# Kernel tuning notes

Hardware: AMD Instinct MI355X
Metric: run time of the kernel (lower is better)

## Reference

```python
import jax, jax.numpy as jnp
import numpy as np

D_MODEL = 1024
H = 4
DK = 128   # head_qk_dim (key_dim=512)
DV = 256   # head_v_dim (value_dim=1024)
EPS = 1e-5
SCALE = DK ** -0.5


def setup_inputs() -> dict:
    key = jax.random.key(0)
    ks = jax.random.split(key, 8)
    w = lambda k, i, o: jax.random.normal(k, (i, o), jnp.float32) * (2.0 ** -2.5) * (6.0 / (i + o)) ** 0.5 * 2
    return {
        "x": jax.random.normal(ks[0], (2, 4096, D_MODEL), jnp.float32),
        "Wq": w(ks[1], D_MODEL, H * DK),
        "Wk": w(ks[2], D_MODEL, H * DK),
        "Wv": w(ks[3], D_MODEL, H * DV),
        "Wb": w(ks[4], D_MODEL, H),
        "Wg": w(ks[5], D_MODEL, H * DV),
        "Wo": w(ks[6], H * DV, D_MODEL),
        "norm_w": jnp.ones((DV,), jnp.float32),
    }


def _delta_rule(q, k, v, beta):
    """Delta-rule linear attention. q,k: [b,n,h,dk], v: [b,n,h,dv], beta: [b,n,h].
    S_t = S_{t-1} + k_t (beta_t * (v_t - k_t^T S_{t-1}))^T ; o_t = q_t^T S_t."""
    b = q.shape[0]
    # time-major for scan: [n,b,h,*]
    qt = jnp.moveaxis(q, 1, 0)
    kt = jnp.moveaxis(k, 1, 0)
    vt = jnp.moveaxis(v, 1, 0)
    bt = jnp.moveaxis(beta, 1, 0)
    S0 = jnp.zeros((b, H, DK, DV), q.dtype)

    def step(S, inp):
        q_t, k_t, v_t, b_t = inp
        pred = jnp.einsum('bhk,bhkv->bhv', k_t, S)          # current memory readout
        delta = (v_t - pred) * b_t[..., None]                # beta-scaled error
        S = S + k_t[..., :, None] * delta[..., None, :]      # rank-1 update [b,h,dk,dv]
        o_t = jnp.einsum('bhk,bhkv->bhv', q_t, S)
        return S, o_t

    _, o = jax.lax.scan(step, S0, (qt, kt, vt, bt))          # o: [n,b,h,dv]
    return jnp.moveaxis(o, 0, 1)                             # [b,n,h,dv]


def reference(x, Wq, Wk, Wv, Wb, Wg, Wo, norm_w):
    b, n, _ = x.shape
    q = (x @ Wq).reshape(b, n, H, DK)
    k = (x @ Wk).reshape(b, n, H, DK)
    v = (x @ Wv).reshape(b, n, H, DV)
    beta = jax.nn.sigmoid(x @ Wb)                            # [b,n,h]
    # L2-normalize keys (delta-rule kernels assume unit-norm k) and scale q
    k = k * jax.lax.rsqrt(jnp.sum(k * k, axis=-1, keepdims=True) + 1e-12)
    q = q * SCALE
    o = _delta_rule(q, k, v, beta)                           # [b,n,h,dv]
    # FusedRMSNormSwishGate over head_v_dim
    g = (x @ Wg).reshape(b, n, H, DV)
    o = o * jax.lax.rsqrt(jnp.mean(o * o, axis=-1, keepdims=True) + EPS) * norm_w
    o = o * (g * jax.nn.sigmoid(g))                          # swish gate
    return o.reshape(b, n, H * DV) @ Wo
```

## Files before the change

kernel.cpp:

```cpp
#include <hip/hip_runtime.h>
#include <hip/hip_bf16.h>
#include <stdint.h>
#include <stddef.h>

typedef __attribute__((ext_vector_type(8))) short short8v;
typedef __attribute__((ext_vector_type(4))) float f32x4;
typedef unsigned short us;

__device__ __forceinline__ float bf2f(unsigned short u) {
    return __uint_as_float(((unsigned int)u) << 16);
}
__device__ __forceinline__ unsigned short f2bf(float f) {
    unsigned int x = __float_as_uint(f);
    x += 0x7fffu + ((x >> 16) & 1u);
    return (unsigned short)(x >> 16);
}
__device__ __forceinline__ unsigned int cvtpk(float lo, float hi) {
    unsigned int r;
    asm("v_cvt_pk_bf16_f32 %0, %1, %2" : "=v"(r) : "v"(lo), "v"(hi));
    return r;
}

#define NTOK 8192
#define DM   1024
#define NPROJ 3072
#define SEQ  4096
#define NCHUNK 64
#define SCQ 0.08838834764831845f

#define GLDS16(g, l) __builtin_amdgcn_global_load_lds( \
    (const __attribute__((address_space(1))) void*)(g), \
    (__attribute__((address_space(3))) void*)(l), 16, 0, 0)

__device__ __forceinline__ void bar_lgkm() {
    asm volatile("s_waitcnt lgkmcnt(0)" ::: "memory");
    __builtin_amdgcn_s_barrier();
    __builtin_amdgcn_sched_barrier(0);
}

__device__ __forceinline__ int sw16(int row, int k) {
    int u = k >> 3;
    int us_ = (u & 8) | ((u ^ row) & 7);
    return row * 128 + us_ * 8 + (k & 7);
}
__device__ __forceinline__ int sw8(int row, int k) {
    int u = k >> 3;
    int us_ = (u ^ row) & 7;
    return row * 64 + us_ * 8 + (k & 7);
}
__device__ __forceinline__ int sw128(int row, int k) {
    int u = k >> 3;
    return row * 128 + ((u ^ row) & 15) * 8 + (k & 7);
}
__device__ __forceinline__ int sw64(int row, int k) {
    int u = k >> 3;
    return row * 64 + ((u ^ row) & 7) * 8 + (k & 7);
}
__device__ __forceinline__ int sw64b(int row, int k) {
    int u = k >> 3;
    return row * 64 + ((u ^ row ^ (row >> 3)) & 7) * 8 + (k & 7);
}
__device__ __forceinline__ int swU(int t, int j) {
    int jj = j & 127, u = jj >> 3;
    int us_ = (u & 8) | ((u ^ t) & 7);
    return t * 256 + (j >> 7) * 128 + us_ * 8 + (jj & 7);
}
__device__ __forceinline__ int swU128(int t, int jj) {
    int u = jj >> 3;
    int us_ = (u & 8) | ((u ^ t) & 7);
    return t * 128 + us_ * 8 + (jj & 7);
}

__global__ __launch_bounds__(256) void prep(
    const float* __restrict__ x, us* __restrict__ xb,
    const float* __restrict__ Wb, float* __restrict__ beta,
    const float* __restrict__ Wq, const float* __restrict__ Wk,
    const float* __restrict__ Wv, const float* __restrict__ Wg,
    const float* __restrict__ Wo, us* __restrict__ WT, us* __restrict__ WoT)
{
    __shared__ float smem[64 * 65];
    int tid = threadIdx.x;
    int bid = blockIdx.x;

    if (bid < 4096) {
        int i = bid * 256 + tid;
        int tok = i >> 7;
        int kb = (i >> 3) & 15;
        int u = i & 7;
        int ko = kb * 64 + ((u ^ (tok & 7)) * 8);
        const float4* src = (const float4*)(x + (size_t)tok * 1024 + ko);
        float4 v0 = src[0], v1 = src[1];
        uint4 o;
        o.x = cvtpk(v0.x, v0.y); o.y = cvtpk(v0.z, v0.w);
        o.z = cvtpk(v1.x, v1.y); o.w = cvtpk(v1.z, v1.w);
        *(uint4*)(xb + (size_t)i * 8) = o;
        const float4* wbv = (const float4*)Wb;
        float xs[8] = {v0.x, v0.y, v0.z, v0.w, v1.x, v1.y, v1.z, v1.w};
        float4 s = {0.f, 0.f, 0.f, 0.f};
        #pragma unroll
        for (int e = 0; e < 8; e++) {
            float4 w = wbv[ko + e];
            s.x += xs[e] * w.x; s.y += xs[e] * w.y;
            s.z += xs[e] * w.z; s.w += xs[e] * w.w;
        }
        *(float4*)&smem[tid * 4] = s;
        __syncthreads();
        if (tid < 8) {
            int tp = tid >> 2, h = tid & 3;
            float acc = 0.f;
            for (int j = 0; j < 128; j++) acc += smem[(tp * 128 + j) * 4 + h];
            beta[(size_t)(bid * 2 + tp) * 4 + h] = 1.f / (1.f + __expf(-acc));
        }
        return;
    }

    int lb = bid - 4096;
    const float* srcw; us* dst; int N;
    if (lb < 128)      { srcw = Wq; dst = WT;                    N = 512;  }
    else if (lb < 256) { srcw = Wk; dst = WT + (size_t)512 * DM;  N = 512;  lb -= 128; }
    else if (lb < 512) { srcw = Wv; dst = WT + (size_t)1024 * DM; N = 1024; lb -= 256; }
    else if (lb < 768) { srcw = Wg; dst = WT + (size_t)2048 * DM; N = 1024; lb -= 512; }
    else               { srcw = Wo; dst = WoT;                   N = 1024; lb -= 768; }
    int nbx = N >> 6;
    int n0 = (lb % nbx) * 64, k0 = (lb / nbx) * 64;
    float (*tl)[65] = (float(*)[65])smem;
    int tr = tid >> 6, tc = tid & 63;
    #pragma unroll
    for (int i2 = 0; i2 < 16; i2++) {
        int kk = 4 * i2 + tr;
        tl[kk][tc] = srcw[(size_t)(k0 + kk) * N + n0 + tc];
    }
    __syncthreads();
    int n = tid >> 2, seg = (tid & 3) * 16;
    short8v a, b;
    #pragma unroll
    for (int e = 0; e < 8; e++) {
        a[e] = (short)f2bf(tl[seg + e][n]);
        b[e] = (short)f2bf(tl[seg + 8 + e][n]);
    }
    int n_ = n0 + n;
    int o1 = (tid & 3) * 2, o2_ = o1 + 1;
    us* d = dst + (size_t)n_ * DM + k0;
    *(short8v*)(d + (o1 ^ (n_ & 7)) * 8) = a;
    *(short8v*)(d + (o2_ ^ (n_ & 7)) * 8) = b;
}

template<int OUT_F32>
__global__ __launch_bounds__(256) void gemm_bt(
    const us* __restrict__ A, const us* __restrict__ BT,
    void* __restrict__ C, int M, int N, int K)
{
    __shared__ us As[2][128 * 64];
    __shared__ us Bs[2][128 * 64];
    int tid = threadIdx.x;
    int wave = tid >> 6, lane = tid & 63;
    int wr = (wave >> 1) * 64, wc = (wave & 1) * 64;
    int fr = lane & 15, fq = lane >> 4;
    int nbx = gridDim.x, nwg = nbx * gridDim.y;
    int wg = blockIdx.y * nbx + blockIdx.x;
    int cpx = nwg >> 3;
    wg = (wg & 7) * cpx + (wg >> 3);
    int m0 = (wg % nbx) * 128, n0 = (wg / nbx) * 128;

    f32x4 acc[4][4];
    #pragma unroll
    for (int i = 0; i < 4; i++)
        #pragma unroll
        for (int j = 0; j < 4; j++) acc[i][j] = (f32x4){0.f, 0.f, 0.f, 0.f};

    int rl = lane >> 3, ul = lane & 7;

    auto issue = [&](int k0, int bufi) {
        #pragma unroll
        for (int i = 0; i < 4; i++) {
            int row = wave * 32 + i * 8 + rl;
            GLDS16(&A[(size_t)(m0 + row) * K + k0 + ul * 8], &As[bufi][(wave * 32 + i * 8) * 64]);
            GLDS16(&BT[(size_t)(n0 + row) * K + k0 + ul * 8], &Bs[bufi][(wave * 32 + i * 8) * 64]);
        }
    };

    int NT = K >> 6;
    issue(0, 0);
    if (NT > 1) issue(64, 1);

    for (int t = 0; t < NT; t++) {
        if (t + 1 < NT) asm volatile("s_waitcnt vmcnt(8)" ::: "memory");
        else            asm volatile("s_waitcnt vmcnt(0)" ::: "memory");
        __builtin_amdgcn_sched_barrier(0);
        __builtin_amdgcn_s_barrier();
        __builtin_amdgcn_sched_barrier(0);
        const us* as = As[t & 1];
        const us* bs = Bs[t & 1];
        #pragma unroll
        for (int kk = 0; kk < 2; kk++) {
            short8v a[4], b[4];
            #pragma unroll
            for (int i = 0; i < 4; i++) {
                int ra = wr + i * 16 + fr;
                a[i] = *(const short8v*)&as[ra * 64 + ((4 * kk + fq) ^ (ra & 7)) * 8];
                int rb = wc + i * 16 + fr;
                b[i] = *(const short8v*)&bs[rb * 64 + ((4 * kk + fq) ^ (rb & 7)) * 8];
            }
            #pragma unroll
            for (int i = 0; i < 4; i++)
                #pragma unroll
                for (int j = 0; j < 4; j++)
                    acc[i][j] = __builtin_amdgcn_mfma_f32_16x16x32_bf16(a[i], b[j], acc[i][j], 0, 0, 0);
        }
        bar_lgkm();
        if (t + 2 < NT) issue((t + 2) * 64, t & 1);
    }

    #pragma unroll
    for (int i = 0; i < 4; i++)
        #pragma unroll
        for (int j = 0; j < 4; j++)
            #pragma unroll
            for (int t = 0; t < 4; t++) {
                int row = m0 + wr + i * 16 + fq * 4 + t;
                int col = n0 + wc + j * 16 + fr;
                float val = acc[i][j][t];
                if (OUT_F32) ((float*)C)[(size_t)row * N + col] = val;
                else ((us*)C)[(size_t)row * N + col] = f2bf(val);
            }
}

__global__ __launch_bounds__(256) void chunk_pre(
    const us* __restrict__ QKVG, const float* __restrict__ beta,
    us* __restrict__ Wbuf, us* __restrict__ Ubuf,
    us* __restrict__ Kbuf, us* __restrict__ KTbuf)
{
    __shared__ us Ks[8192];
    __shared__ us KTs[8192];
    __shared__ us VT[8192];
    __shared__ us Tb[4096];
    __shared__ float Af[64][64];
    __shared__ float betas[64];

    int c = blockIdx.x, bh = blockIdx.y;
    int b = bh >> 2, h = bh & 3;
    int tid = threadIdx.x;
    int wv = tid >> 6, ln = tid & 63;
    int fr = ln & 15, fq = ln >> 4;
    int tok0 = b * SEQ + c * 64;
    size_t cb = (size_t)bh * NCHUNK + c;

    #pragma unroll
    for (int r = 0; r < 4; r++) {
        int idx = tid + 256 * r;
        int t = idx >> 4, u = idx & 15;
        short8v kv = *(const short8v*)(QKVG + (size_t)(tok0 + t) * NPROJ + 512 + h * 128 + u * 8);
        *(short8v*)(Ks + sw16(t, u * 8)) = kv;
    }
    if (tid < 64) betas[tid] = beta[(size_t)(tok0 + tid) * 4 + h];
    __syncthreads();

    {
        int t = tid >> 2, p = tid & 3;
        short8v v[4];
        float ss = 0.f;
        #pragma unroll
        for (int uu = 0; uu < 4; uu++) {
            v[uu] = *(const short8v*)(Ks + sw16(t, (p * 4 + uu) * 8));
            #pragma unroll
            for (int e = 0; e < 8; e++) {
                float f = bf2f((unsigned short)v[uu][e]);
                ss += f * f;
            }
        }
        ss += __shfl_xor(ss, 1);
        ss += __shfl_xor(ss, 2);
        float rn = rsqrtf(ss + 1e-12f);
        #pragma unroll
        for (int uu = 0; uu < 4; uu++) {
            short8v o;
            #pragma unroll
            for (int e = 0; e < 8; e++)
                o[e] = (short)f2bf(bf2f((unsigned short)v[uu][e]) * rn);
            *(short8v*)(Ks + sw16(t, (p * 4 + uu) * 8)) = o;
        }
    }
    __syncthreads();

    {
        f32x4 aacc[4];
        #pragma unroll
        for (int jt = 0; jt < 4; jt++) aacc[jt] = (f32x4){0.f, 0.f, 0.f, 0.f};
        #pragma unroll
        for (int ks = 0; ks < 4; ks++) {
            short8v ak = *(const short8v*)(Ks + sw16(16 * wv + fr, 32 * ks + 8 * fq));
            #pragma unroll
            for (int jt = 0; jt < 4; jt++) {
                short8v bk = *(const short8v*)(Ks + sw16(16 * jt + fr, 32 * ks + 8 * fq));
                aacc[jt] = __builtin_amdgcn_mfma_f32_16x16x32_bf16(ak, bk, aacc[jt], 0, 0, 0);
            }
        }
        #pragma unroll
        for (int jt = 0; jt < 4; jt++)
            #pragma unroll
            for (int r = 0; r < 4; r++) {
                int t = 16 * wv + 4 * fq + r, s = 16 * jt + fr;
                if (s < t) Af[t][s] = betas[t] * aacc[jt][r];
            }
    }
    __syncthreads();

    if (wv == 0) {
        int cc = ln;
        for (int tb = 0; tb < 8; tb++) {
            int base = tb * 8;
            float xs[8];
            #pragma unroll
            for (int i = 0; i < 8; i++) {
                int t = base + i;
                float v = Af[t][cc];
                #pragma unroll
                for (int s = 0; s < i; s++)
                    v += Af[t][base + s] * xs[s];
                float xt = (cc < t) ? -v : 0.f;
                xs[i] = xt;
                if (cc < t) Af[t][cc] = xt;
            }
            for (int r = base + 8; r < 64; r += 2) {
                float u0 = 0.f, u1 = 0.f;
                #pragma unroll
                for (int s = 0; s < 8; s++) {
                    float a0 = Af[r][base + s];
                    float a1 = Af[r + 1][base + s];
                    u0 += a0 * xs[s];
                    u1 += a1 * xs[s];
                }
                Af[r][cc] += u0;
                Af[r + 1][cc] += u1;
            }
        }
    } else {
        int q = tid - 64;
        for (int g = q; g < 1024; g += 192) {
            int t = g >> 4, u = g & 15;
            short8v kv = *(const short8v*)(Ks + sw16(t, u * 8));
            #pragma unroll
            for (int e = 0; e < 8; e++)
                KTs[sw64b(u * 8 + e, t)] = (unsigned short)kv[e];
        }
        for (int g = q; g < 1024; g += 192) {
            int t = g >> 4, jg = g & 15;
            short8v vv = *(const short8v*)(QKVG + (size_t)(tok0 + t) * NPROJ + 1024 + h * 256 + jg * 8);
            #pragma unroll
            for (int e = 0; e < 8; e++)
                VT[sw64b(jg * 8 + e, t)] = (unsigned short)vv[e];
        }
    }
    __syncthreads();

    {
        #pragma unroll
        for (int i = 0; i < 4; i++) {
            int idx = tid + 256 * i;
            int t = idx >> 4, u = idx & 15;
            short8v kv = *(const short8v*)(Ks + sw16(t, u * 8));
            *(short8v*)(Kbuf + cb * 8192 + t * 128 + (size_t)(((u ^ t) & 15) * 8)) = kv;
        }
        #pragma unroll
        for (int i = 0; i < 16; i++) {
            int idx = tid + 256 * i;
            int t = idx >> 6, s = idx & 63;
            float tv = (s < t) ? Af[t][s] : (s == t ? 1.f : 0.f);
            Tb[sw8(t, s)] = f2bf(tv * betas[s]);
        }
        #pragma unroll
        for (int i = 0; i < 4; i++) {
            int idx = tid + 256 * i;
            *(short8v*)(KTbuf + cb * 8192 + (size_t)idx * 8) =
                *(const short8v*)(KTs + (size_t)idx * 8);
        }
    }
    __syncthreads();

    {
        f32x4 wacc[8], uacc[8];
        #pragma unroll
        for (int jt = 0; jt < 8; jt++) {
            wacc[jt] = (f32x4){0.f, 0.f, 0.f, 0.f};
            uacc[jt] = (f32x4){0.f, 0.f, 0.f, 0.f};
        }
        #pragma unroll
        for (int ks = 0; ks < 2; ks++) {
            short8v at = *(const short8v*)(Tb + sw8(16 * wv + fr, 32 * ks + 8 * fq));
            #pragma unroll
            for (int jt = 0; jt < 8; jt++) {
                short8v bk = *(const short8v*)(KTs + sw64b(16 * jt + fr, 32 * ks + 8 * fq));
                wacc[jt] = __builtin_amdgcn_mfma_f32_16x16x32_bf16(at, bk, wacc[jt], 0, 0, 0);
                short8v bv = *(const short8v*)(VT + sw64b(16 * jt + fr, 32 * ks + 8 * fq));
                uacc[jt] = __builtin_amdgcn_mfma_f32_16x16x32_bf16(at, bv, uacc[jt], 0, 0, 0);
            }
        }
        #pragma unroll
        for (int jt = 0; jt < 8; jt++)
            #pragma unroll
            for (int r = 0; r < 4; r++) {
                int t = 16 * wv + 4 * fq + r, d = 16 * jt + fr;
                Wbuf[cb * 8192 + (d >> 6) * 4096 + sw64(t, d & 63)] = f2bf(-wacc[jt][r]);
                Ubuf[cb * 16384 + swU(t, d)] = f2bf(uacc[jt][r]);
            }
    }
    __syncthreads();

    #pragma unroll
    for (int i = 0; i < 4; i++) {
        int g = tid + 256 * i;
        int t = g >> 4, jg = g & 15;
        short8v vv = *(const short8v*)(QKVG + (size_t)(tok0 + t) * NPROJ + 1024 + h * 256 + 128 + jg * 8);
        #pragma unroll
        for (int e = 0; e < 8; e++)
            VT[sw64b(jg * 8 + e, t)] = (unsigned short)vv[e];
    }
    __syncthreads();
    {
        f32x4 uacc[8];
        #pragma unroll
        for (int jt = 0; jt < 8; jt++) uacc[jt] = (f32x4){0.f, 0.f, 0.f, 0.f};
        #pragma unroll
        for (int ks = 0; ks < 2; ks++) {
            short8v at = *(const short8v*)(Tb + sw8(16 * wv + fr, 32 * ks + 8 * fq));
            #pragma unroll
            for (int jt = 0; jt < 8; jt++) {
                short8v bv = *(const short8v*)(VT + sw64b(16 * jt + fr, 32 * ks + 8 * fq));
                uacc[jt] = __builtin_amdgcn_mfma_f32_16x16x32_bf16(at, bv, uacc[jt], 0, 0, 0);
            }
        }
        #pragma unroll
        for (int jt = 0; jt < 8; jt++)
            #pragma unroll
            for (int r = 0; r < 4; r++) {
                int t = 16 * wv + 4 * fq + r, j = 16 * jt + fr;
                Ubuf[cb * 16384 + swU(t, 128 + j)] = f2bf(uacc[jt][r]);
            }
    }
}

#define SCW 0
#define SCKT 8192
#define SCU 16384
#define SCBUF 17408
#define SSTB (2 * SCBUF)
#define SDTB (2 * SCBUF + 2048)

__global__ __launch_bounds__(256, 1) void fused_scan_qg(
    const us* __restrict__ xb, const us* __restrict__ WT, us* __restrict__ QKVG,
    const us* __restrict__ Wbuf, const us* __restrict__ Ubuf,
    const us* __restrict__ KTbuf, us* __restrict__ Sbuf)
{
    extern __shared__ us lds[];
    int tid = threadIdx.x;

    if (blockIdx.x < 128) {
        if (tid >= 128) {
            for (int c = 0; c < NCHUNK; c++) __builtin_amdgcn_s_barrier();
            return;
        }
        int wv = tid >> 6, ln = tid & 63;
        int fr = ln & 15, fq = ln >> 4;
        int sl = blockIdx.x >> 3;
        int j0 = sl * 16;
        int bh = blockIdx.x & 7;

        short8v id0;
        #pragma unroll
        for (int e = 0; e < 8; e++)
            id0[e] = (short)((8 * fq + e == fr) ? 0x3F80 : 0);

        f32x4 sacc[4];
        #pragma unroll
        for (int i = 0; i < 4; i++) sacc[i] = (f32x4){0.f, 0.f, 0.f, 0.f};

        us* ST = lds + SSTB + wv * 1024;

        auto issue = [&](int c1) {
            size_t cb = (size_t)bh * NCHUNK + c1;
            us* dst = lds + (c1 & 1) * SCBUF;
            const us* Wc = Wbuf + cb * 8192 + wv * 4096;
            const us* Kc = KTbuf + cb * 8192 + wv * 4096;
            #pragma unroll
            for (int i = 0; i < 8; i++) {
                GLDS16(Wc + i * 512 + ln * 8, dst + SCW + wv * 4096 + i * 512);
                GLDS16(Kc + i * 512 + ln * 8, dst + SCKT + wv * 4096 + i * 512);
            }
            if (wv) {
                const us* Uc = Ubuf + cb * 16384;
                #pragma unroll
                for (int i = 0; i < 2; i++) {
                    int t = i * 32 + (ln >> 1);
                    GLDS16(Uc + swU(t, j0 + (ln & 1) * 8), dst + SCU + i * 512);
                }
            }
        };

        issue(0);

        for (int c = 0; c < NCHUNK; c++) {
            const us* ba = lds + (c & 1) * SCBUF;
            us* DTw = lds + SDTB + (c & 1) * 2048 + wv * 1024;
            const us* DTr = lds + SDTB + (c & 1) * 2048;
            size_t sb = ((size_t)bh * NCHUNK + c) * 32768 + sl * 2048 + wv * 1024;

            #pragma unroll
            for (int dt = 0; dt < 4; dt++) {
                uint2 w;
                w.x = cvtpk(sacc[dt][0], sacc[dt][1]);
                w.y = cvtpk(sacc[dt][2], sacc[dt][3]);
                int dl = 16 * dt + 4 * fq;
                int off = fr * 64 + (((dl >> 3) ^ fr) & 7) * 8 + (dl & 7);
                *(uint2*)&ST[off] = w;
                *(uint2*)(Sbuf + sb + off) = w;
            }
            if (c + 1 < NCHUNK) issue(c + 1);
            if (c + 1 < NCHUNK) {
                if (wv) asm volatile("s_waitcnt vmcnt(22)" ::: "memory");
                else    asm volatile("s_waitcnt vmcnt(20)" ::: "memory");
            } else {
                asm volatile("s_waitcnt vmcnt(4)" ::: "memory");
            }
            __builtin_amdgcn_sched_barrier(0);

            f32x4 dacc[4];
            #pragma unroll
            for (int tt = 0; tt < 4; tt++) dacc[tt] = (f32x4){0.f, 0.f, 0.f, 0.f};
            #pragma unroll
            for (int kc = 0; kc < 2; kc++) {
                short8v bs = *(const short8v*)&ST[fr * 64 + (((4 * kc + fq) ^ fr) & 7) * 8];
                #pragma unroll
                for (int tt = 0; tt < 4; tt++) {
                    short8v aw = *(const short8v*)&ba[SCW + wv * 4096 + sw64(16 * tt + fr, 32 * kc + 8 * fq)];
                    dacc[tt] = __builtin_amdgcn_mfma_f32_16x16x32_bf16(aw, bs, dacc[tt], 0, 0, 0);
                }
            }
            if (wv) {
                #pragma unroll
                for (int tt = 0; tt < 4; tt++) {
                    short8v au = *(const short8v*)&ba[SCU + (16 * tt + fr) * 16 + 8 * (fq & 1)];
                    dacc[tt] = __builtin_amdgcn_mfma_f32_16x16x32_bf16(au, id0, dacc[tt], 0, 0, 0);
                }
            }
            #pragma unroll
            for (int tt = 0; tt < 4; tt++) {
                uint2 w;
                w.x = cvtpk(dacc[tt][0], dacc[tt][1]);
                w.y = cvtpk(dacc[tt][2], dacc[tt][3]);
                int tl = 16 * tt + 4 * fq;
                *(uint2*)&DTw[fr * 64 + (((tl >> 3) ^ fr) & 7) * 8 + (tl & 7)] = w;
            }
            bar_lgkm();
            #pragma unroll
            for (int kc2 = 0; kc2 < 2; kc2++) {
                int o = fr * 64 + (((4 * kc2 + fq) ^ fr) & 7) * 8;
                short8v bd0 = *(const short8v*)&DTr[o];
                short8v bd1 = *(const short8v*)&DTr[1024 + o];
                #pragma unroll
                for (int dt = 0; dt < 4; dt++) {
                    short8v ak = *(const short8v*)&ba[SCKT + sw64b(64 * wv + 16 * dt + fr, 32 * kc2 + 8 * fq)];
                    sacc[dt] = __builtin_amdgcn_mfma_f32_16x16x32_bf16(ak, bd0, sacc[dt], 0, 0, 0);
                    sacc[dt] = __builtin_amdgcn_mfma_f32_16x16x32_bf16(ak, bd1, sacc[dt], 0, 0, 0);
                }
            }
        }
        return;
    }

    {
        us* As = lds;
        us* Bs = lds + 8192;
        int wave = tid >> 6, lane = tid & 63;
        int wr = (wave >> 1) * 64, wc = (wave & 1) * 64;
        int fr = lane & 15, fq = lane >> 4;
        int wg = blockIdx.x - 128;
        wg = (wg & 7) * 96 + (wg >> 3);
        int m0 = (wg % 64) * 128;
        int ntile = wg / 64;
        int n0 = ntile * 128 + (ntile >= 4 ? 1536 : 0);

        f32x4 acc[4][4];
        #pragma unroll
        for (int i = 0; i < 4; i++)
            #pragma unroll
            for (int j = 0; j < 4; j++) acc[i][j] = (f32x4){0.f, 0.f, 0.f, 0.f};

        int rl = lane >> 3, ul = lane & 7;

        for (int k0 = 0; k0 < DM; k0 += 64) {
            #pragma unroll
            for (int i = 0; i < 4; i++) {
                int row = wave * 32 + i * 8 + rl;
                GLDS16(&xb[(size_t)(m0 + row) * DM + k0 + ul * 8], As + (wave * 32 + i * 8) * 64);
                GLDS16(&WT[(size_t)(n0 + row) * DM + k0 + ul * 8], Bs + (wave * 32 + i * 8) * 64);
            }
            __syncthreads();
            #pragma unroll
            for (int kk = 0; kk < 2; kk++) {
                short8v a[4], b[4];
                #pragma unroll
                for (int i = 0; i < 4; i++) {
                    int ra = wr + i * 16 + fr;
                    a[i] = *(const short8v*)&As[ra * 64 + ((4 * kk + fq) ^ (ra & 7)) * 8];
                    int rb = wc + i * 16 + fr;
                    b[i] = *(const short8v*)&Bs[rb * 64 + ((4 * kk + fq) ^ (rb & 7)) * 8];
                }
                #pragma unroll
                for (int i = 0; i < 4; i++)
                    #pragma unroll
                    for (int j = 0; j < 4; j++)
                        acc[i][j] = __builtin_amdgcn_mfma_f32_16x16x32_bf16(a[i], b[j], acc[i][j], 0, 0, 0);
            }
            __syncthreads();
        }
        #pragma unroll
        for (int i = 0; i < 4; i++)
            #pragma unroll
            for (int j = 0; j < 4; j++)
                #pragma unroll
                for (int t = 0; t < 4; t++) {
                    int row = m0 + wr + i * 16 + fq * 4 + t;
                    int col = n0 + wc + j * 16 + fr;
                    QKVG[(size_t)row * NPROJ + col] = f2bf(acc[i][j][t]);
                }
    }
}

#define K2_W 0
#define K2_P 8192
#define K2_U 12288
#define K2_S 20480
#define K2_Q 36864
#define K2_DT 45056
#define K2_K 53248

__global__ __launch_bounds__(256, 1) void out_k(
    const us* __restrict__ QKVG, const us* __restrict__ Wbuf,
    const us* __restrict__ Ubuf, const us* __restrict__ Kbuf,
    const us* __restrict__ Sbuf, us* __restrict__ Ob)
{
    extern __shared__ us lds[];
    int tid = threadIdx.x;
    int wv = tid >> 6, ln = tid & 63;
    int fr = ln & 15, fq = ln >> 4;
    int c = blockIdx.x;
    int bh = blockIdx.y >> 1, jh = blockIdx.y & 1;
    int b = bh >> 2, h = bh & 3;
    int tok0 = b * SEQ + c * 64;
    size_t cb = (size_t)bh * NCHUNK + c;

    short8v id0, id1;
    #pragma unroll
    for (int e = 0; e < 8; e++) {
        id0[e] = (short)((8 * fq + e == fr) ? 0x3F80 : 0);
        id1[e] = (short)((8 * fq + e == fr + 16) ? 0x3F80 : 0);
    }

    #pragma unroll
    for (int i = 0; i < 4; i++) {
        int q = (i * 4 + wv) * 512 + ln * 8;
        GLDS16(Wbuf + cb * 8192 + q, lds + K2_W + (i * 4 + wv) * 512);
    }
    #pragma unroll
    for (int i = 0; i < 4; i++) {
        int q = (i * 4 + wv) * 512 + ln * 8;
        GLDS16(Kbuf + cb * 8192 + q, lds + K2_K + (i * 4 + wv) * 512);
    }
    #pragma unroll
    for (int i = 0; i < 4; i++) {
        int q = (i * 4 + wv) * 512 + ln * 8;
        int t = q >> 7, r = q & 127;
        GLDS16(Ubuf + cb * 16384 + t * 256 + jh * 128 + r, lds + K2_U + (i * 4 + wv) * 512);
    }
    size_t sbase = cb * 32768 + (size_t)jh * 16384;
    #pragma unroll
    for (int i = 0; i < 8; i++) {
        int q = (i * 4 + wv) * 512 + ln * 8;
        GLDS16(Sbuf + sbase + q, lds + K2_S + (i * 4 + wv) * 512);
    }
    short8v qv[4];
    #pragma unroll
    for (int i = 0; i < 4; i++) {
        int idx = tid + 256 * i;
        int t = idx >> 4, u = idx & 15;
        qv[i] = *(const short8v*)(QKVG + (size_t)(tok0 + t) * NPROJ + h * 128 + u * 8);
    }
    #pragma unroll
    for (int i = 0; i < 4; i++) {
        int idx = tid + 256 * i;
        int t = idx >> 4, u = idx & 15;
        *(short8v*)&lds[K2_Q + sw128(t, u * 8)] = qv[i];
    }
    __syncthreads();

    f32x4 dacc[8], oacc[8];
    #pragma unroll
    for (int jt = 0; jt < 8; jt++) {
        dacc[jt] = (f32x4){0.f, 0.f, 0.f, 0.f};
        oacc[jt] = (f32x4){0.f, 0.f, 0.f, 0.f};
    }
    #pragma unroll
    for (int ks = 0; ks < 4; ks++) {
        short8v aw = *(const short8v*)&lds[K2_W + (ks >> 1) * 4096
            + sw64(16 * wv + fr, (ks & 1) * 32 + 8 * fq)];
        short8v aq = *(const short8v*)&lds[K2_Q + sw128(16 * wv + fr, 32 * ks + 8 * fq)];
        #pragma unroll
        for (int jt = 0; jt < 8; jt++) {
            short8v bs = *(const short8v*)&lds[K2_S + jt * 2048 + (ks >> 1) * 1024
                + fr * 64 + ((((ks & 1) * 4 + fq) ^ fr) & 7) * 8];
            dacc[jt] = __builtin_amdgcn_mfma_f32_16x16x32_bf16(aw, bs, dacc[jt], 0, 0, 0);
            oacc[jt] = __builtin_amdgcn_mfma_f32_16x16x32_bf16(aq, bs, oacc[jt], 0, 0, 0);
        }
    }
    #pragma unroll
    for (int ju = 0; ju < 4; ju++) {
        short8v au = *(const short8v*)&lds[K2_U + swU128(16 * wv + fr, 32 * ju + 8 * fq)];
        dacc[2 * ju + 0] = __builtin_amdgcn_mfma_f32_16x16x32_bf16(au, id0, dacc[2 * ju + 0], 0, 0, 0);
        dacc[2 * ju + 1] = __builtin_amdgcn_mfma_f32_16x16x32_bf16(au, id1, dacc[2 * ju + 1], 0, 0, 0);
    }
    {
        f32x4 pacc[4];
        #pragma unroll
        for (int jt2 = 0; jt2 < 4; jt2++) pacc[jt2] = (f32x4){0.f, 0.f, 0.f, 0.f};
        #pragma unroll
        for (int ks = 0; ks < 4; ks++) {
            short8v aq = *(const short8v*)&lds[K2_Q + sw128(16 * wv + fr, 32 * ks + 8 * fq)];
            #pragma unroll
            for (int jt2 = 0; jt2 < 4; jt2++) {
                short8v bk = *(const short8v*)&lds[K2_K + sw128(16 * jt2 + fr, 32 * ks + 8 * fq)];
                pacc[jt2] = __builtin_amdgcn_mfma_f32_16x16x32_bf16(aq, bk, pacc[jt2], 0, 0, 0);
            }
        }
        #pragma unroll
        for (int jt2 = 0; jt2 < 4; jt2++)
            #pragma unroll
            for (int r = 0; r < 4; r++) {
                int t = 16 * wv + 4 * fq + r, s = 16 * jt2 + fr;
                float val = (s <= t) ? pacc[jt2][r] * SCQ : 0.f;
                lds[K2_P + sw64(t, s)] = f2bf(val);
            }
    }
    #pragma unroll
    for (int jt = 0; jt < 8; jt++)
        #pragma unroll
        for (int r = 0; r < 4; r++) oacc[jt][r] *= SCQ;
    #pragma unroll
    for (int jt = 0; jt < 8; jt++) {
        int j = 16 * jt + fr;
        int t0 = 16 * wv + 4 * fq;
        uint2 w;
        w.x = cvtpk(dacc[jt][0], dacc[jt][1]);
        w.y = cvtpk(dacc[jt][2], dacc[jt][3]);
        *(uint2*)&lds[K2_DT + sw64(j, t0)] = w;
    }
    bar_lgkm();

    #pragma unroll
    for (int ks = 0; ks < 2; ks++) {
        short8v ap = *(const short8v*)&lds[K2_P + sw64(16 * wv + fr, 32 * ks + 8 * fq)];
        #pragma unroll
        for (int jt = 0; jt < 8; jt++) {
            short8v bd = *(const short8v*)&lds[K2_DT + sw64(16 * jt + fr, 32 * ks + 8 * fq)];
            oacc[jt] = __builtin_amdgcn_mfma_f32_16x16x32_bf16(ap, bd, oacc[jt], 0, 0, 0);
        }
    }
    us* ob = Ob + (size_t)tok0 * 1024 + h * 256 + jh * 128;
    #pragma unroll
    for (int jt = 0; jt < 8; jt++)
        #pragma unroll
        for (int r = 0; r < 4; r++) {
            int t = 16 * wv + 4 * fq + r;
            ob[(size_t)t * 1024 + 16 * jt + fr] = f2bf(oacc[jt][r]);
        }
}

__global__ __launch_bounds__(256) void gate_norm(const us* __restrict__ Ob,
                                                 const us* __restrict__ QKVG,
                                                 const float* __restrict__ norm_w,
                                                 us* __restrict__ o2)
{
    int gid = blockIdx.x * 4 + (threadIdx.x >> 6);
    int ln = threadIdx.x & 63;
    int tok = gid >> 2, h = gid & 3;
    size_t base = (size_t)tok * 1024 + h * 256 + ln * 4;
    uint2 ov = *(const uint2*)&Ob[base];
    float o0 = bf2f((us)ov.x), o1 = bf2f((us)(ov.x >> 16));
    float o2v = bf2f((us)ov.y), o3 = bf2f((us)(ov.y >> 16));
    float ss = o0 * o0 + o1 * o1 + o2v * o2v + o3 * o3;
    #pragma unroll
    for (int off = 32; off; off >>= 1) ss += __shfl_xor(ss, off);
    float r = rsqrtf(ss * (1.0f / 256.0f) + 1e-5f);
    uint2 gv = *(const uint2*)&QKVG[(size_t)tok * NPROJ + 2048 + h * 256 + ln * 4];
    float g0 = bf2f((us)gv.x), g1 = bf2f((us)(gv.x >> 16));
    float g2 = bf2f((us)gv.y), g3 = bf2f((us)(gv.y >> 16));
    float4 nw = *(const float4*)&norm_w[ln * 4];
    float r0 = o0 * r * nw.x * (g0 / (1.f + __expf(-g0)));
    float r1 = o1 * r * nw.y * (g1 / (1.f + __expf(-g1)));
    float r2 = o2v * r * nw.z * (g2 / (1.f + __expf(-g2)));
    float r3 = o3 * r * nw.w * (g3 / (1.f + __expf(-g3)));
    uint2 w;
    w.x = cvtpk(r0, r1);
    w.y = cvtpk(r2, r3);
    int u = h * 32 + (ln >> 1);
    size_t dsto = (size_t)tok * 1024 + (size_t)(u >> 3) * 64
                + (size_t)(((u & 7) ^ (tok & 7)) * 8) + (ln & 1) * 4;
    *(uint2*)&o2[dsto] = w;
}

extern "C" void kernel_launch(void* const* d_in, const int* in_sizes, int n_in,
                              void* d_out, int out_size, void* d_ws, size_t ws_size,
                              hipStream_t stream) {
    const float* x      = (const float*)d_in[0];
    const float* Wq     = (const float*)d_in[1];
    const float* Wk     = (const float*)d_in[2];
    const float* Wv     = (const float*)d_in[3];
    const float* Wb     = (const float*)d_in[4];
    const float* Wg     = (const float*)d_in[5];
    const float* Wo     = (const float*)d_in[6];
    const float* norm_w = (const float*)d_in[7];
    float* out = (float*)d_out;

    char* ws = (char*)d_ws;
    us*    xb   = (us*)(ws + 0);
    us*    Ob   = (us*)(ws + 0);
    us*    WT   = (us*)(ws + 16777216);
    us*    KTbuf= (us*)(ws + 23068672);
    us*    QKVG = (us*)(ws + 31457280);
    float* beta = (float*)(ws + 81788928);
    us*    Wbuf = (us*)(ws + 81920000);
    us*    Ubuf = (us*)(ws + 90308608);
    us*    o2   = (us*)(ws + 90308608);
    us*    Kbuf = (us*)(ws + 107085824);
    us*    WoT  = (us*)(ws + 115474432);
    us*    Sbuf = (us*)(ws + 117571584);

    (void)hipFuncSetAttribute((const void*)fused_scan_qg,
                              hipFuncAttributeMaxDynamicSharedMemorySize, 81920);
    (void)hipFuncSetAttribute((const void*)out_k,
                              hipFuncAttributeMaxDynamicSharedMemorySize, 122880);

    prep<<<5120, 256, 0, stream>>>(x, xb, Wb, beta, Wq, Wk, Wv, Wg, Wo, WT, WoT);
    gemm_bt<0><<<dim3(64, 12), 256, 0, stream>>>(xb, WT + (size_t)512 * DM,
                                                 (void*)(QKVG + 512), NTOK, NPROJ, DM);
    chunk_pre<<<dim3(NCHUNK, 8), 256, 0, stream>>>(QKVG, beta, Wbuf, Ubuf, Kbuf, KTbuf);
    fused_scan_qg<<<896, 256, 81920, stream>>>(xb, WT, QKVG, Wbuf, Ubuf, KTbuf, Sbuf);
    out_k<<<dim3(NCHUNK, 16), 256, 122880, stream>>>(QKVG, Wbuf, Ubuf, Kbuf, Sbuf, Ob);
    gate_norm<<<NTOK, 256, 0, stream>>>(Ob, QKVG, norm_w, o2);
    gemm_bt<1><<<dim3(64, 8), 256, 0, stream>>>(o2, WoT, (void*)out, NTOK, DM, DM);
}
```

Before: 234.1 us.

## Fuse RMSNorm swish-gate into chunk output kernel with 512-thread blocks

Merges the two value-half blocks of out_k into one 512-thread block per (chunk, head), so W, K and the Q·K^T intra-chunk scores are loaded and computed once rather than twice. The per-token RMSNorm and swish gate, previously a separate gate_norm kernel, now run in the same block: output rows are staged as fp32 in LDS and the gate values are pulled in with async copies. This removes one launch and the bf16 Ob round trip through global memory, and normalises from fp32 instead of rounded values. Q fragments and U are now read directly from global memory into registers, and LDS use grows to 136 KB, so only one block can run per CU.

Measured after the change: 229.2 us (median of 2 runs). 2.1% less time.

```diff
diff --git a/kernel.cpp b/kernel.cpp
--- a/kernel.cpp
+++ b/kernel.cpp
@@ -64,11 +64,6 @@
     int jj = j & 127, u = jj >> 3;
     int us_ = (u & 8) | ((u ^ t) & 7);
     return t * 256 + (j >> 7) * 128 + us_ * 8 + (jj & 7);
-}
-__device__ __forceinline__ int swU128(int t, int jj) {
-    int u = jj >> 3;
-    int us_ = (u & 8) | ((u ^ t) & 7);
-    return t * 128 + us_ * 8 + (jj & 7);
 }
 
 __global__ __launch_bounds__(256) void prep(
@@ -626,25 +621,26 @@
     }
 }
 
-#define K2_W 0
-#define K2_P 8192
-#define K2_U 12288
-#define K2_S 20480
-#define K2_Q 36864
-#define K2_DT 45056
-#define K2_K 53248
-
-__global__ __launch_bounds__(256, 1) void out_k(
+#define OKW 0
+#define OKK 8192
+#define OKP 16384
+#define OKS 20480
+#define OKDT 53248
+
+__global__ __launch_bounds__(512, 1) void out_k(
     const us* __restrict__ QKVG, const us* __restrict__ Wbuf,
     const us* __restrict__ Ubuf, const us* __restrict__ Kbuf,
-    const us* __restrict__ Sbuf, us* __restrict__ Ob)
+    const us* __restrict__ Sbuf, const float* __restrict__ norm_w,
+    us* __restrict__ o2)
 {
     extern __shared__ us lds[];
     int tid = threadIdx.x;
-    int wv = tid >> 6, ln = tid & 63;
+    int wvg = (tid >> 6) & 3;
+    int jh = tid >> 8;
+    int ln = tid & 63;
     int fr = ln & 15, fq = ln >> 4;
     int c = blockIdx.x;
-    int bh = blockIdx.y >> 1, jh = blockIdx.y & 1;
+    int bh = blockIdx.y;
     int b = bh >> 2, h = bh & 3;
     int tok0 = b * SEQ + c * 64;
     size_t cb = (size_t)bh * NCHUNK + c;
@@ -657,40 +653,21 @@
     }
 
     #pragma unroll
-    for (int i = 0; i < 4; i++) {
-        int q = (i * 4 + wv) * 512 + ln * 8;
-        GLDS16(Wbuf + cb * 8192 + q, lds + K2_W + (i * 4 + wv) * 512);
-    }
-    #pragma unroll
-    for (int i = 0; i < 4; i++) {
-        int q = (i * 4 + wv) * 512 + ln * 8;
-        GLDS16(Kbuf + cb * 8192 + q, lds + K2_K + (i * 4 + wv) * 512);
-    }
-    #pragma unroll
-    for (int i = 0; i < 4; i++) {
-        int q = (i * 4 + wv) * 512 + ln * 8;
-        int t = q >> 7, r = q & 127;
-        GLDS16(Ubuf + cb * 16384 + t * 256 + jh * 128 + r, lds + K2_U + (i * 4 + wv) * 512);
-    }
-    size_t sbase = cb * 32768 + (size_t)jh * 16384;
+    for (int i = 0; i < 2; i++) {
+        int q = (tid + 512 * i) * 8;
+        GLDS16(Wbuf + cb * 8192 + q, lds + OKW + q);
+        GLDS16(Kbuf + cb * 8192 + q, lds + OKK + q);
+    }
     #pragma unroll
     for (int i = 0; i < 8; i++) {
-        int q = (i * 4 + wv) * 512 + ln * 8;
-        GLDS16(Sbuf + sbase + q, lds + K2_S + (i * 4 + wv) * 512);
-    }
-    short8v qv[4];
-    #pragma unroll
-    for (int i = 0; i < 4; i++) {
-        int idx = tid + 256 * i;
-        int t = idx >> 4, u = idx & 15;
-        qv[i] = *(const short8v*)(QKVG + (size_t)(tok0 + t) * NPROJ + h * 128 + u * 8);
-    }
-    #pragma unroll
-    for (int i = 0; i < 4; i++) {
-        int idx = tid + 256 * i;
-        int t = idx >> 4, u = idx & 15;
-        *(short8v*)&lds[K2_Q + sw128(t, u * 8)] = qv[i];
-    }
+        int q = (tid + 512 * i) * 8;
+        GLDS16(Sbuf + cb * 32768 + q, lds + OKS + q);
+    }
+    short8v qf[4];
+    #pragma unroll
+    for (int ks = 0; ks < 4; ks++)
+        qf[ks] = *(const short8v*)(QKVG + (size_t)(tok0 + 16 * wvg + fr) * NPROJ
+                                   + h * 128 + ks * 32 + fq * 8);
     __syncthreads();
 
     f32x4 dacc[8], oacc[8];
@@ -701,12 +678,12 @@
     }
     #pragma unroll
     for (int ks = 0; ks < 4; ks++) {
-        short8v aw = *(const short8v*)&lds[K2_W + (ks >> 1) * 4096
-            + sw64(16 * wv + fr, (ks & 1) * 32 + 8 * fq)];
-        short8v aq = *(const short8v*)&lds[K2_Q + sw128(16 * wv + fr, 32 * ks + 8 * fq)];
+        short8v aw = *(const short8v*)&lds[OKW + (ks >> 1) * 4096
+            + sw64(16 * wvg + fr, (ks & 1) * 32 + 8 * fq)];
+        short8v aq = qf[ks];
         #pragma unroll
         for (int jt = 0; jt < 8; jt++) {
-            short8v bs = *(const short8v*)&lds[K2_S + jt * 2048 + (ks >> 1) * 1024
+            short8v bs = *(const short8v*)&lds[OKS + jh * 16384 + jt * 2048 + (ks >> 1) * 1024
                 + fr * 64 + ((((ks & 1) * 4 + fq) ^ fr) & 7) * 8];
             dacc[jt] = __builtin_amdgcn_mfma_f32_16x16x32_bf16(aw, bs, dacc[jt], 0, 0, 0);
             oacc[jt] = __builtin_amdgcn_mfma_f32_16x16x32_bf16(aq, bs, oacc[jt], 0, 0, 0);
@@ -714,20 +691,21 @@
     }
     #pragma unroll
     for (int ju = 0; ju < 4; ju++) {
-        short8v au = *(const short8v*)&lds[K2_U + swU128(16 * wv + fr, 32 * ju + 8 * fq)];
+        short8v au = *(const short8v*)(Ubuf + cb * 16384
+            + swU(16 * wvg + fr, jh * 128 + 32 * ju + 8 * fq));
         dacc[2 * ju + 0] = __builtin_amdgcn_mfma_f32_16x16x32_bf16(au, id0, dacc[2 * ju + 0], 0, 0, 0);
         dacc[2 * ju + 1] = __builtin_amdgcn_mfma_f32_16x16x32_bf16(au, id1, dacc[2 * ju + 1], 0, 0, 0);
     }
-    {
+    if (jh == 0) {
         f32x4 pacc[4];
         #pragma unroll
         for (int jt2 = 0; jt2 < 4; jt2++) pacc[jt2] = (f32x4){0.f, 0.f, 0.f, 0.f};
         #pragma unroll
         for (int ks = 0; ks < 4; ks++) {
-            short8v aq = *(const short8v*)&lds[K2_Q + sw128(16 * wv + fr, 32 * ks + 8 * fq)];
+            short8v aq = qf[ks];
             #pragma unroll
             for (int jt2 = 0; jt2 < 4; jt2++) {
-                short8v bk = *(const short8v*)&lds[K2_K + sw128(16 * jt2 + fr, 32 * ks + 8 * fq)];
+                short8v bk = *(const short8v*)&lds[OKK + sw128(16 * jt2 + fr, 32 * ks + 8 * fq)];
                 pacc[jt2] = __builtin_amdgcn_mfma_f32_16x16x32_bf16(aq, bk, pacc[jt2], 0, 0, 0);
             }
         }
@@ -735,9 +713,9 @@
         for (int jt2 = 0; jt2 < 4; jt2++)
             #pragma unroll
             for (int r = 0; r < 4; r++) {
-                int t = 16 * wv + 4 * fq + r, s = 16 * jt2 + fr;
+                int t = 16 * wvg + 4 * fq + r, s = 16 * jt2 + fr;
                 float val = (s <= t) ? pacc[jt2][r] * SCQ : 0.f;
-                lds[K2_P + sw64(t, s)] = f2bf(val);
+                lds[OKP + sw64(t, s)] = f2bf(val);
             }
     }
     #pragma unroll
@@ -746,65 +724,78 @@
         for (int r = 0; r < 4; r++) oacc[jt][r] *= SCQ;
     #pragma unroll
     for (int jt = 0; jt < 8; jt++) {
-        int j = 16 * jt + fr;
-        int t0 = 16 * wv + 4 * fq;
+        int jg = jh * 128 + 16 * jt + fr;
+        int t0 = 16 * wvg + 4 * fq;
         uint2 w;
         w.x = cvtpk(dacc[jt][0], dacc[jt][1]);
         w.y = cvtpk(dacc[jt][2], dacc[jt][3]);
-        *(uint2*)&lds[K2_DT + sw64(j, t0)] = w;
+        *(uint2*)&lds[OKDT + sw64(jg, t0)] = w;
     }
     bar_lgkm();
 
     #pragma unroll
     for (int ks = 0; ks < 2; ks++) {
-        short8v ap = *(const short8v*)&lds[K2_P + sw64(16 * wv + fr, 32 * ks + 8 * fq)];
+        short8v ap = *(const short8v*)&lds[OKP + sw64(16 * wvg + fr, 32 * ks + 8 * fq)];
         #pragma unroll
         for (int jt = 0; jt < 8; jt++) {
-            short8v bd = *(const short8v*)&lds[K2_DT + sw64(16 * jt + fr, 32 * ks + 8 * fq)];
+            short8v bd = *(const short8v*)&lds[OKDT + sw64(jh * 128 + 16 * jt + fr, 32 * ks + 8 * fq)];
             oacc[jt] = __builtin_amdgcn_mfma_f32_16x16x32_bf16(ap, bd, oacc[jt], 0, 0, 0);
         }
     }
-    us* ob = Ob + (size_t)tok0 * 1024 + h * 256 + jh * 128;
+    __syncthreads();
+
+    float* OSf = (float*)lds;
     #pragma unroll
     for (int jt = 0; jt < 8; jt++)
         #pragma unroll
         for (int r = 0; r < 4; r++) {
-            int t = 16 * wv + 4 * fq + r;
-            ob[(size_t)t * 1024 + 16 * jt + fr] = f2bf(oacc[jt][r]);
-        }
-}
-
-__global__ __launch_bounds__(256) void gate_norm(const us* __restrict__ Ob,
-                                                 const us* __restrict__ QKVG,
-                                                 const float* __restrict__ norm_w,
-                                                 us* __restrict__ o2)
-{
-    int gid = blockIdx.x * 4 + (threadIdx.x >> 6);
-    int ln = threadIdx.x & 63;
-    int tok = gid >> 2, h = gid & 3;
-    size_t base = (size_t)tok * 1024 + h * 256 + ln * 4;
-    uint2 ov = *(const uint2*)&Ob[base];
-    float o0 = bf2f((us)ov.x), o1 = bf2f((us)(ov.x >> 16));
-    float o2v = bf2f((us)ov.y), o3 = bf2f((us)(ov.y >> 16));
-    float ss = o0 * o0 + o1 * o1 + o2v * o2v + o3 * o3;
-    #pragma unroll
-    for (int off = 32; off; off >>= 1) ss += __shfl_xor(ss, off);
-    float r = rsqrtf(ss * (1.0f / 256.0f) + 1e-5f);
-    uint2 gv = *(const uint2*)&QKVG[(size_t)tok * NPROJ + 2048 + h * 256 + ln * 4];
-    float g0 = bf2f((us)gv.x), g1 = bf2f((us)(gv.x >> 16));
-    float g2 = bf2f((us)gv.y), g3 = bf2f((us)(gv.y >> 16));
-    float4 nw = *(const float4*)&norm_w[ln * 4];
-    float r0 = o0 * r * nw.x * (g0 / (1.f + __expf(-g0)));
-    float r1 = o1 * r * nw.y * (g1 / (1.f + __expf(-g1)));
-    float r2 = o2v * r * nw.z * (g2 / (1.f + __expf(-g2)));
-    float r3 = o3 * r * nw.w * (g3 / (1.f + __expf(-g3)));
-    uint2 w;
-    w.x = cvtpk(r0, r1);
-    w.y = cvtpk(r2, r3);
-    int u = h * 32 + (ln >> 1);
-    size_t dsto = (size_t)tok * 1024 + (size_t)(u >> 3) * 64
-                + (size_t)(((u & 7) ^ (tok & 7)) * 8) + (ln & 1) * 4;
-    *(uint2*)&o2[dsto] = w;
+            int t = 16 * wvg + 4 * fq + r;
+            OSf[t * 260 + jh * 128 + 16 * jt + fr] = oacc[jt][r];
+        }
+    #pragma unroll
+    for (int l = 0; l < 4; l++) {
+        int idx = tid + 512 * l;
+        int tt = idx >> 5, ccol = (idx & 31) * 8;
+        GLDS16(QKVG + (size_t)(tok0 + tt) * NPROJ + 2048 + h * 256 + ccol,
+               lds + OKDT + idx * 8);
+    }
+    __syncthreads();
+
+    {
+        int t = tid >> 3, p = tid & 7;
+        int tok = tok0 + t;
+        f32x4 ov[8];
+        float ssum = 0.f;
+        #pragma unroll
+        for (int g = 0; g < 8; g++) {
+            ov[g] = *(const f32x4*)&OSf[t * 260 + 32 * p + 4 * g];
+            ssum += ov[g][0] * ov[g][0] + ov[g][1] * ov[g][1]
+                  + ov[g][2] * ov[g][2] + ov[g][3] * ov[g][3];
+        }
+        ssum += __shfl_xor(ssum, 1);
+        ssum += __shfl_xor(ssum, 2);
+        ssum += __shfl_xor(ssum, 4);
+        float rr = rsqrtf(ssum * (1.0f / 256.0f) + 1e-5f);
+        #pragma unroll
+        for (int g = 0; g < 8; g++) {
+            int j0g = 32 * p + 4 * g;
+            uint2 gv = *(const uint2*)&lds[OKDT + t * 256 + j0g];
+            float4 nw = *(const float4*)&norm_w[j0g];
+            float g0 = bf2f((us)gv.x), g1 = bf2f((us)(gv.x >> 16));
+            float g2 = bf2f((us)gv.y), g3 = bf2f((us)(gv.y >> 16));
+            float r0 = ov[g][0] * rr * nw.x * (g0 / (1.f + __expf(-g0)));
+            float r1 = ov[g][1] * rr * nw.y * (g1 / (1.f + __expf(-g1)));
+            float r2 = ov[g][2] * rr * nw.z * (g2 / (1.f + __expf(-g2)));
+            float r3 = ov[g][3] * rr * nw.w * (g3 / (1.f + __expf(-g3)));
+            uint2 w;
+            w.x = cvtpk(r0, r1);
+            w.y = cvtpk(r2, r3);
+            int u = h * 32 + (j0g >> 3);
+            size_t dsto = (size_t)tok * 1024 + (size_t)(u >> 3) * 64
+                        + (size_t)(((u & 7) ^ (tok & 7)) * 8) + (j0g & 7);
+            *(uint2*)&o2[dsto] = w;
+        }
+    }
 }
 
 extern "C" void kernel_launch(void* const* d_in, const int* in_sizes, int n_in,
@@ -822,14 +813,13 @@
 
     char* ws = (char*)d_ws;
     us*    xb   = (us*)(ws + 0);
-    us*    Ob   = (us*)(ws + 0);
+    us*    o2   = (us*)(ws + 0);
     us*    WT   = (us*)(ws + 16777216);
     us*    KTbuf= (us*)(ws + 23068672);
     us*    QKVG = (us*)(ws + 31457280);
     float* beta = (float*)(ws + 81788928);
     us*    Wbuf = (us*)(ws + 81920000);
     us*    Ubuf = (us*)(ws + 90308608);
-    us*    o2   = (us*)(ws + 90308608);
     us*    Kbuf = (us*)(ws + 107085824);
     us*    WoT  = (us*)(ws + 115474432);
     us*    Sbuf = (us*)(ws + 117571584);
@@ -837,14 +827,13 @@
     (void)hipFuncSetAttribute((const void*)fused_scan_qg,
                               hipFuncAttributeMaxDynamicSharedMemorySize, 81920);
     (void)hipFuncSetAttribute((const void*)out_k,
-                              hipFuncAttributeMaxDynamicSharedMemorySize, 122880);
+                              hipFuncAttributeMaxDynamicSharedMemorySize, 139264);
 
     prep<<<5120, 256, 0, stream>>>(x, xb, Wb, beta, Wq, Wk, Wv, Wg, Wo, WT, WoT);
     gemm_bt<0><<<dim3(64, 12), 256, 0, stream>>>(xb, WT + (size_t)512 * DM,
                                                  (void*)(QKVG + 512), NTOK, NPROJ, DM);
     chunk_pre<<<dim3(NCHUNK, 8), 256, 0, stream>>>(QKVG, beta, Wbuf, Ubuf, Kbuf, KTbuf);
     fused_scan_qg<<<896, 256, 81920, stream>>>(xb, WT, QKVG, Wbuf, Ubuf, KTbuf, Sbuf);
-    out_k<<<dim3(NCHUNK, 16), 256, 122880, stream>>>(QKVG, Wbuf, Ubuf, Kbuf, Sbuf, Ob);
-    gate_norm<<<NTOK, 256, 0, stream>>>(Ob, QKVG, norm_w, o2);
+    out_k<<<dim3(NCHUNK, 8), 512, 139264, stream>>>(QKVG, Wbuf, Ubuf, Kbuf, Sbuf, norm_w, o2);
     gemm_bt<1><<<dim3(64, 8), 256, 0, stream>>>(o2, WoT, (void*)out, NTOK, DM, DM);
 }
```
